# Performance work log

Hardware: AMD Instinct MI355X
Metric: run time of the kernel (lower is better)

## Reference

```python
import jax, jax.numpy as jnp
import numpy as np

N, NS, CIN, COUT, S = 65536, 16, 64, 64, 8
MID = COUT  # mid_planes = out_planes // 1
EPS = 1e-5


def _bn(t, g, b):
    # BatchNorm1d in training mode: normalize per channel over (points, neighbors)
    m = jnp.mean(t, axis=(0, 1), keepdims=True)
    v = jnp.var(t, axis=(0, 1), keepdims=True)
    return (t - m) * jax.lax.rsqrt(v + EPS) * g + b


def setup_inputs() -> dict:
    key = jax.random.key(0)
    ks = jax.random.split(key, 16)

    def w(k, shape, fan_in):
        return (jax.random.normal(k, shape, jnp.float32) / np.sqrt(fan_in)).astype(jnp.float32)

    return {
        "p": jax.random.uniform(ks[0], (N, 3), jnp.float32),
        "x": jax.random.normal(ks[1], (N, CIN), jnp.float32),
        "idx": jax.random.randint(ks[2], (N, NS), 0, N, jnp.int32),
        # q/k/v linears
        "Wq": w(ks[3], (CIN, MID), CIN), "bq": jnp.zeros((MID,), jnp.float32),
        "Wk": w(ks[4], (CIN, MID), CIN), "bk": jnp.zeros((MID,), jnp.float32),
        "Wv": w(ks[5], (CIN, COUT), CIN), "bv": jnp.zeros((COUT,), jnp.float32),
        # linear_p: Linear(3,3) -> BN(3) -> ReLU -> Linear(3,out)
        "Wp1": w(ks[6], (3, 3), 3), "bp1": jnp.zeros((3,), jnp.float32),
        "gp": jnp.ones((3,), jnp.float32), "bp_bn": jnp.zeros((3,), jnp.float32),
        "Wp2": w(ks[7], (3, COUT), 3), "bp2": jnp.zeros((COUT,), jnp.float32),
        # linear_w: BN(mid)->ReLU->Linear(mid,mid//s)->BN->ReLU->Linear(mid//s,mid//s)
        "gw1": jnp.ones((MID,), jnp.float32), "bw1_bn": jnp.zeros((MID,), jnp.float32),
        "Ww1": w(ks[8], (MID, MID // S), MID), "bw1": jnp.zeros((MID // S,), jnp.float32),
        "gw2": jnp.ones((MID // S,), jnp.float32), "bw2_bn": jnp.zeros((MID // S,), jnp.float32),
        "Ww2": w(ks[9], (MID // S, MID // S), MID // S), "bw2": jnp.zeros((MID // S,), jnp.float32),
    }


def reference(p, x, idx, Wq, bq, Wk, bk, Wv, bv, Wp1, bp1, gp, bp_bn, Wp2, bp2,
              gw1, bw1_bn, Ww1, bw1, gw2, bw2_bn, Ww2, bw2):
    # per-point projections
    xq = x @ Wq + bq                       # [N, MID]
    xk = x @ Wk + bk                       # [N, MID]
    xv = x @ Wv + bv                       # [N, COUT]
    # queryandgroup: gather neighbor features + relative xyz
    rel_p = p[idx] - p[:, None, :]         # [N, NS, 3]
    xk_g = xk[idx]                         # [N, NS, MID]
    xv_g = xv[idx]                         # [N, NS, COUT]
    # linear_p MLP on relative positions
    pr = rel_p @ Wp1 + bp1
    pr = jax.nn.relu(_bn(pr, gp, bp_bn))
    pr = pr @ Wp2 + bp2                    # [N, NS, COUT]
    # subtractive attention logits (out//mid == 1, so p_r sum is identity)
    w = xk_g - xq[:, None, :] + pr         # [N, NS, MID]
    # linear_w MLP
    w = jax.nn.relu(_bn(w, gw1, bw1_bn))
    w = w @ Ww1 + bw1                      # [N, NS, MID//S]
    w = jax.nn.relu(_bn(w, gw2, bw2_bn))
    w = w @ Ww2 + bw2                      # [N, NS, COUT//S]
    w = jax.nn.softmax(w, axis=1)          # softmax over neighbors
    # grouped weighted aggregation with shared attention planes
    n, ns, c = xv_g.shape
    out = ((xv_g + pr).reshape(n, ns, S, c // S) * w[:, :, None, :]).sum(1)
    return out.reshape(n, c)
```

## Files before the change

### kernel.cpp

```cpp
#include <hip/hip_runtime.h>

typedef unsigned short u16;
typedef __attribute__((ext_vector_type(8))) short bf16x8;
typedef __attribute__((ext_vector_type(2))) float f32x2;
typedef __attribute__((ext_vector_type(4))) float f32x4;

#define NPTS 65536
#define MTOT 1048576
#define M2TOT 131072
#define EPSb 1e-5f

#define XQ_OFF  0u
#define T_OFF   4194304u
#define ST_OFF  15728640u
#define XK_US   31457792u
#define XV_US   35652096u
#define WTQ_US  14680064u
#define WT1_US  14692352u

__device__ __forceinline__ float bf2f(u16 h) {
    return __uint_as_float(((unsigned)h) << 16);
}
__device__ __forceinline__ u16 f2bf(float f) {
    unsigned u = __float_as_uint(f);
    u += 0x7fffu + ((u >> 16) & 1u);
    return (u16)(u >> 16);
}
__device__ __forceinline__ unsigned cvt_pk_bf16(float lo, float hi) {
    unsigned r;
    asm("v_cvt_pk_bf16_f32 %0, %1, %2" : "=v"(r) : "v"(lo), "v"(hi));
    return r;
}
__device__ __forceinline__ bf16x8 pack_bf8(const float4 lo, const float4 hi) {
    union { bf16x8 v; unsigned u[4]; } r;
    r.u[0] = cvt_pk_bf16(lo.x, lo.y);
    r.u[1] = cvt_pk_bf16(lo.z, lo.w);
    r.u[2] = cvt_pk_bf16(hi.x, hi.y);
    r.u[3] = cvt_pk_bf16(hi.z, hi.w);
    return r.v;
}

struct BN2C {
    f32x2 A2[4], D[4], W0[4], W1[4], W2[4];
};
__device__ __forceinline__ void bn2c_build(
    BN2C& c, const int kbase, const float* __restrict__ ws,
    const float* __restrict__ gw1, const float* __restrict__ bw1_bn,
    const float* __restrict__ bp2, const float* __restrict__ Wp2)
{
    const float invM2 = 1.0f / (float)M2TOT;
#pragma unroll
    for (int j = 0; j < 4; ++j) {
        float a2[2], d[2], w0[2], w1[2], w2[2];
#pragma unroll
        for (int h = 0; h < 2; ++h) {
            const int k = kbase + 2 * j + h;
            const float mean = ws[ST_OFF + 6 + k] * invM2;
            const float var  = ws[ST_OFF + 70 + k] * invM2 - mean * mean;
            const float A2 = gw1[k] * rsqrtf(var + EPSb);
            const float B2 = bw1_bn[k] - mean * A2;
            a2[h] = A2; d[h] = fmaf(A2, bp2[k], B2);
            w0[h] = A2 * Wp2[k]; w1[h] = A2 * Wp2[64 + k]; w2[h] = A2 * Wp2[128 + k];
        }
        c.A2[j] = f32x2{a2[0], a2[1]}; c.D[j] = f32x2{d[0], d[1]};
        c.W0[j] = f32x2{w0[0], w0[1]}; c.W1[j] = f32x2{w1[0], w1[1]};
        c.W2[j] = f32x2{w2[0], w2[1]};
    }
}
__device__ __forceinline__ bf16x8 build_frag(
    const BN2C& c, const f32x2 t0v, const f32x2 t1v, const f32x2 t2v,
    const uint4 g, const float4 xlo, const float4 xhi)
{
    union { bf16x8 v; unsigned u[4]; } r;
    const unsigned gu[4] = { g.x, g.y, g.z, g.w };
    const f32x2 xp[4] = { {xlo.x, xlo.y}, {xlo.z, xlo.w}, {xhi.x, xhi.y}, {xhi.z, xhi.w} };
#pragma unroll
    for (int j = 0; j < 4; ++j) {
        f32x2 gf;
        gf.x = __uint_as_float(gu[j] << 16);
        gf.y = __uint_as_float(gu[j] & 0xffff0000u);
        f32x2 v = c.D[j] - c.A2[j] * xp[j];
        v = v + t0v * c.W0[j];
        v = v + t1v * c.W1[j];
        v = v + t2v * c.W2[j];
        v = v + c.A2[j] * gf;
        r.u[j] = cvt_pk_bf16(fmaxf(v.x, 0.0f), fmaxf(v.y, 0.0f));
    }
    return r.v;
}

__global__ __launch_bounds__(256) void k0_mom_tab(
    const float* __restrict__ p, const int* __restrict__ idx,
    const float* __restrict__ Wq, const float* __restrict__ Wk,
    const float* __restrict__ Wv, const float* __restrict__ Ww1,
    const float* __restrict__ Wp1, const float* __restrict__ bp1,
    float* __restrict__ ws)
{
    u16* wsu = (u16*)ws;
    __shared__ float sred[6];
    const int tid = threadIdx.x;
    const int gid = blockIdx.x * 256 + tid;
    if (tid < 6) sred[tid] = 0.0f;
    __syncthreads();

    if (gid < 12288) {
        const float* W = (gid < 4096) ? Wq : ((gid < 8192) ? Wk : Wv);
        const int rem = gid & 4095;
        const int n = rem >> 6, c = rem & 63;
        wsu[WTQ_US + (unsigned)gid] = f2bf(W[c * 64 + n]);
    } else if (gid < 12800) {
        const int rem = gid - 12288;
        const int c = rem >> 6, r = rem & 63;
        wsu[WT1_US + (unsigned)rem] = f2bf(Ww1[r * 8 + c]);
    }

    const int base = blockIdx.x * 128;
    const float w00 = Wp1[0], w01 = Wp1[1], w02 = Wp1[2];
    const float w10 = Wp1[3], w11 = Wp1[4], w12 = Wp1[5];
    const float w20 = Wp1[6], w21 = Wp1[7], w22 = Wp1[8];
    const float c0 = bp1[0], c1 = bp1[1], c2 = bp1[2];
    float s0 = 0, s1 = 0, s2 = 0, q0 = 0, q1 = 0, q2 = 0;
#pragma unroll
    for (int m = 0; m < 8; ++m) {
        const int pl = tid + m * 256;
        const int n  = base + (pl >> 4);
        const unsigned gpair = (unsigned)(base * 16 + pl);
        const int nb = idx[gpair];
        const float r0 = p[nb * 3 + 0] - p[n * 3 + 0];
        const float r1 = p[nb * 3 + 1] - p[n * 3 + 1];
        const float r2 = p[nb * 3 + 2] - p[n * 3 + 2];
        const float t0 = c0 + r0 * w00 + r1 * w10 + r2 * w20;
        const float t1 = c1 + r0 * w01 + r1 * w11 + r2 * w21;
        const float t2 = c2 + r0 * w02 + r1 * w12 + r2 * w22;
        s0 += t0; s1 += t1; s2 += t2;
        q0 += t0 * t0; q1 += t1 * t1; q2 += t2 * t2;
    }
    atomicAdd(&sred[0], s0); atomicAdd(&sred[1], s1); atomicAdd(&sred[2], s2);
    atomicAdd(&sred[3], q0); atomicAdd(&sred[4], q1); atomicAdd(&sred[5], q2);
    __syncthreads();
    if (tid < 6) atomicAdd(&ws[ST_OFF + tid], sred[tid]);
}

__global__ __launch_bounds__(256) void k1_proj(
    const float* __restrict__ p, const float* __restrict__ x, const int* __restrict__ idx,
    const float* __restrict__ bq, const float* __restrict__ bk, const float* __restrict__ bv,
    const float* __restrict__ Wp1, const float* __restrict__ bp1,
    const float* __restrict__ gp, const float* __restrict__ bp_bn,
    float* __restrict__ ws)
{
    u16* wsu = (u16*)ws;
    const int tid   = threadIdx.x;
    const int lane  = tid & 63;
    const int wid   = tid >> 6;
    const int col16 = lane & 15;
    const int quad  = lane >> 4;

    const float invM = 1.0f / (float)MTOT;
    float A1[3], B1[3];
#pragma unroll
    for (int a = 0; a < 3; ++a) {
        const float mean = ws[ST_OFF + a] * invM;
        const float var  = ws[ST_OFF + 3 + a] * invM - mean * mean;
        const float sc = gp[a] * rsqrtf(var + EPSb);
        A1[a] = sc; B1[a] = bp_bn[a] - mean * sc;
    }

    bf16x8 bf[3][4][2];
#pragma unroll
    for (int M = 0; M < 3; ++M)
#pragma unroll
        for (int t = 0; t < 4; ++t)
#pragma unroll
            for (int h = 0; h < 2; ++h)
                bf[M][t][h] = *(const bf16x8*)&wsu[WTQ_US +
                    (unsigned)(M * 4096 + (t * 16 + col16) * 64 + h * 32 + quad * 8)];

    float bq_t[4], bk_t[4], bv_t[4];
#pragma unroll
    for (int t = 0; t < 4; ++t) {
        bq_t[t] = bq[t * 16 + col16];
        bk_t[t] = bk[t * 16 + col16];
        bv_t[t] = bv[t * 16 + col16];
    }

    float* xq   = ws + XQ_OFF;
    u16*  xkb   = wsu + XK_US;
    u16*  xvb   = wsu + XV_US;

    const int gw = blockIdx.x * 4 + wid;
#pragma unroll
    for (int g = 0; g < 2; ++g) {
        const int n0 = (gw * 2 + g) * 16;
        const float* xrow = x + (unsigned)(n0 + col16) * 64u;
        const float4 fa0 = *(const float4*)&xrow[quad * 8];
        const float4 fa1 = *(const float4*)&xrow[quad * 8 + 4];
        const float4 fb0 = *(const float4*)&xrow[32 + quad * 8];
        const float4 fb1 = *(const float4*)&xrow[32 + quad * 8 + 4];
        const bf16x8 a0 = pack_bf8(fa0, fa1);
        const bf16x8 a1 = pack_bf8(fb0, fb1);

#pragma unroll
        for (int t = 0; t < 4; ++t) {
            f32x4 aq = {0,0,0,0}, ak = {0,0,0,0}, av = {0,0,0,0};
            aq = __builtin_amdgcn_mfma_f32_16x16x32_bf16(a0, bf[0][t][0], aq, 0, 0, 0);
            aq = __builtin_amdgcn_mfma_f32_16x16x32_bf16(a1, bf[0][t][1], aq, 0, 0, 0);
            ak = __builtin_amdgcn_mfma_f32_16x16x32_bf16(a0, bf[1][t][0], ak, 0, 0, 0);
            ak = __builtin_amdgcn_mfma_f32_16x16x32_bf16(a1, bf[1][t][1], ak, 0, 0, 0);
            av = __builtin_amdgcn_mfma_f32_16x16x32_bf16(a0, bf[2][t][0], av, 0, 0, 0);
            av = __builtin_amdgcn_mfma_f32_16x16x32_bf16(a1, bf[2][t][1], av, 0, 0, 0);
#pragma unroll
            for (int r = 0; r < 4; ++r) {
                const unsigned row = (unsigned)(n0 + quad * 4 + r);
                const unsigned o   = row * 64u + (unsigned)(t * 16 + col16);
                xq[o]  = aq[r] + bq_t[t];
                xkb[o] = f2bf(ak[r] + bk_t[t]);
                xvb[o] = f2bf(av[r] + bv_t[t]);
            }
        }
    }

    const int base = blockIdx.x * 128;
    const float w00 = Wp1[0], w01 = Wp1[1], w02 = Wp1[2];
    const float w10 = Wp1[3], w11 = Wp1[4], w12 = Wp1[5];
    const float w20 = Wp1[6], w21 = Wp1[7], w22 = Wp1[8];
    const float c0 = bp1[0], c1 = bp1[1], c2 = bp1[2];
#pragma unroll
    for (int m = 0; m < 8; ++m) {
        const int pl = tid + m * 256;
        const int n  = base + (pl >> 4);
        const unsigned gpair = (unsigned)(base * 16 + pl);
        const int nb = idx[gpair];
        const float r0 = p[nb * 3 + 0] - p[n * 3 + 0];
        const float r1 = p[nb * 3 + 1] - p[n * 3 + 1];
        const float r2 = p[nb * 3 + 2] - p[n * 3 + 2];
        const float t0 = c0 + r0 * w00 + r1 * w10 + r2 * w20;
        const float t1 = c1 + r0 * w01 + r1 * w11 + r2 * w21;
        const float t2 = c2 + r0 * w02 + r1 * w12 + r2 * w22;
        ws[T_OFF + gpair * 3u + 0u] = fmaxf(fmaf(t0, A1[0], B1[0]), 0.0f);
        ws[T_OFF + gpair * 3u + 1u] = fmaxf(fmaf(t1, A1[1], B1[1]), 0.0f);
        ws[T_OFF + gpair * 3u + 2u] = fmaxf(fmaf(t2, A1[2], B1[2]), 0.0f);
    }
}

__global__ __launch_bounds__(256) void k2_bn2(
    const int* __restrict__ idx,
    const float* __restrict__ Wp2, const float* __restrict__ bp2,
    float* __restrict__ ws)
{
    u16* wsu = (u16*)ws;
    __shared__ float ss[64], sq[64];
    const int tid = threadIdx.x;
    const int lane = tid & 63;
    const int gw = blockIdx.x * 4 + (tid >> 6);
    if (tid < 64) { ss[tid] = 0.0f; sq[tid] = 0.0f; }

    const float wp20 = Wp2[lane], wp21 = Wp2[64 + lane], wp22 = Wp2[128 + lane];
    const float bp2c = bp2[lane];
    const float* xq  = ws + XQ_OFF;
    const float* T   = ws + T_OFF;
    const u16*  xkb  = wsu + XK_US;

    float s = 0.0f, q = 0.0f;

    for (int nn = 0; nn < 4; ++nn) {
        const int nu = __builtin_amdgcn_readfirstlane((gw * 4 + nn) * 8);

        const int4* ir4 = (const int4*)(idx + (unsigned)nu * 16u);
        const int4 i0 = ir4[0], i1 = ir4[1], i2 = ir4[2], i3 = ir4[3];
        const int nbs[16] = { i0.x, i0.y, i0.z, i0.w, i1.x, i1.y, i1.z, i1.w,
                              i2.x, i2.y, i2.z, i2.w, i3.x, i3.y, i3.z, i3.w };
        u16 kr[16];
#pragma unroll
        for (int j = 0; j < 16; ++j) kr[j] = xkb[(unsigned)nbs[j] * 64u + lane];

        float tr[48];
        const float4* Tr4 = (const float4*)(T + (unsigned)nu * 48u);
#pragma unroll
        for (int c = 0; c < 12; ++c) {
            const float4 v = Tr4[c];
            tr[4 * c + 0] = v.x; tr[4 * c + 1] = v.y;
            tr[4 * c + 2] = v.z; tr[4 * c + 3] = v.w;
        }
        const float xqc  = xq[(unsigned)nu * 64u + lane];
        const float base = bp2c - xqc;

#pragma unroll
        for (int j = 0; j < 16; ++j) {
            const float prx = base + tr[3 * j + 0] * wp20
                                   + tr[3 * j + 1] * wp21
                                   + tr[3 * j + 2] * wp22;
            const float w0 = bf2f(kr[j]) + prx;
            s += w0; q = fmaf(w0, w0, q);
        }
    }
    __syncthreads();
    atomicAdd(&ss[lane], s); atomicAdd(&sq[lane], q);
    __syncthreads();
    if (tid < 64) {
        atomicAdd(&ws[ST_OFF + 6 + tid], ss[tid]);
        atomicAdd(&ws[ST_OFF + 70 + tid], sq[tid]);
    }
}

__global__ __launch_bounds__(256) void k2b_bn3(
    const int* __restrict__ idx,
    const float* __restrict__ Wp2, const float* __restrict__ bp2,
    const float* __restrict__ gw1, const float* __restrict__ bw1_bn,
    const float* __restrict__ bw1,
    float* __restrict__ ws)
{
    u16* wsu = (u16*)ws;
    __shared__ float s3r[8], q3r[8];
    const int tid   = threadIdx.x;
    const int lane  = tid & 63;
    const int wid   = tid >> 6;
    const int col16 = lane & 15;
    const int quad  = lane >> 4;
    if (tid < 8) { s3r[tid] = 0.0f; q3r[tid] = 0.0f; }
    __syncthreads();

    BN2C cA, cB;
    bn2c_build(cA, quad * 8,      ws, gw1, bw1_bn, bp2, Wp2);
    bn2c_build(cB, 32 + quad * 8, ws, gw1, bw1_bn, bp2, Wp2);

    bf16x8 b0 = {0,0,0,0,0,0,0,0}, b1 = {0,0,0,0,0,0,0,0};
    if (col16 < 8) {
        b0 = *(const bf16x8*)&wsu[WT1_US + (unsigned)(col16 * 64 + quad * 8)];
        b1 = *(const bf16x8*)&wsu[WT1_US + (unsigned)(col16 * 64 + 32 + quad * 8)];
    }
    const float bw1c = (col16 < 8) ? bw1[col16] : 0.0f;

    const float* xq  = ws + XQ_OFF;
    const float* T   = ws + T_OFF;
    const u16*  xkb  = wsu + XK_US;
    const int sg = (blockIdx.x * 4 + wid) * 8;
    float bs = 0.0f, bq2 = 0.0f;

    for (int it = 0; it < 8; ++it) {
        const int nu = __builtin_amdgcn_readfirstlane((sg + it) * 8);

        const int nbv = idx[(unsigned)nu * 16u + (unsigned)col16];
        const u16* grow = xkb + (unsigned)nbv * 64u;
        const uint4 gA = *(const uint4*)(grow + quad * 8);
        const uint4 gB = *(const uint4*)(grow + 32 + quad * 8);

        const float* Trow = T + (unsigned)nu * 48u + (unsigned)col16 * 3u;
        const f32x2 t0v = f32x2{Trow[0], Trow[0]};
        const f32x2 t1v = f32x2{Trow[1], Trow[1]};
        const f32x2 t2v = f32x2{Trow[2], Trow[2]};

        const float* xr = xq + (unsigned)nu * 64u;
        const float4 x0 = *(const float4*)(xr + quad * 8);
        const float4 x1 = *(const float4*)(xr + quad * 8 + 4);
        const float4 x2 = *(const float4*)(xr + 32 + quad * 8);
        const float4 x3 = *(const float4*)(xr + 32 + quad * 8 + 4);

        const bf16x8 a0 = build_frag(cA, t0v, t1v, t2v, gA, x0, x1);
        const bf16x8 a1 = build_frag(cB, t0v, t1v, t2v, gB, x2, x3);

        f32x4 acc = {0.0f, 0.0f, 0.0f, 0.0f};
        acc = __builtin_amdgcn_mfma_f32_16x16x32_bf16(a0, b0, acc, 0, 0, 0);
        acc = __builtin_amdgcn_mfma_f32_16x16x32_bf16(a1, b1, acc, 0, 0, 0);
        if (col16 < 8) {
#pragma unroll
            for (int r = 0; r < 4; ++r) {
                const float o = acc[r] + bw1c;
                bs += o;
                bq2 = fmaf(o, o, bq2);
            }
        }
    }
    if (col16 < 8) {
        atomicAdd(&s3r[col16], bs);
        atomicAdd(&q3r[col16], bq2);
    }
    __syncthreads();
    if (tid < 8) {
        atomicAdd(&ws[ST_OFF + 134 + tid], s3r[tid]);
        atomicAdd(&ws[ST_OFF + 142 + tid], q3r[tid]);
    }
}

__global__ __launch_bounds__(256) void k34_fused(
    const int* __restrict__ idx,
    const float* __restrict__ Wp2, const float* __restrict__ bp2,
    const float* __restrict__ gw1, const float* __restrict__ bw1_bn,
    const float* __restrict__ bw1,
    const float* __restrict__ gw2, const float* __restrict__ bw2_bn,
    const float* __restrict__ Ww2, const float* __restrict__ bw2,
    const float* __restrict__ ws, float* __restrict__ out)
{
    const u16* wsu = (const u16*)ws;
    __shared__ float sv3[4][16][8];
    __shared__ float se[4][16][8];
    const int tid   = threadIdx.x;
    const int lane  = tid & 63;
    const int wid   = tid >> 6;
    const int col16 = lane & 15;
    const int quad  = lane >> 4;
    const int tt    = lane & 7;
    const int j1    = lane >> 3;

    const float invM2 = 1.0f / (float)M2TOT;
    BN2C cA, cB;
    bn2c_build(cA, quad * 8,      ws, gw1, bw1_bn, bp2, Wp2);
    bn2c_build(cB, 32 + quad * 8, ws, gw1, bw1_bn, bp2, Wp2);

    bf16x8 b0 = {0,0,0,0,0,0,0,0}, b1 = {0,0,0,0,0,0,0,0};
    if (col16 < 8) {
        b0 = *(const bf16x8*)&wsu[WT1_US + (unsigned)(col16 * 64 + quad * 8)];
        b1 = *(const bf16x8*)&wsu[WT1_US + (unsigned)(col16 * 64 + 32 + quad * 8)];
    }
    const float bw1c = (col16 < 8) ? bw1[col16] : 0.0f;
    const int   c3    = col16 & 7;
    const float mean3 = ws[ST_OFF + 134 + c3] * invM2;
    const float var3  = ws[ST_OFF + 142 + c3] * invM2 - mean3 * mean3;
    const float A3c   = gw2[c3] * rsqrtf(var3 + EPSb);
    const float B3f   = fmaf(A3c, bw1c, bw2_bn[c3] - mean3 * A3c);
    float ww2c[8];
#pragma unroll
    for (int u = 0; u < 8; ++u) ww2c[u] = Ww2[u * 8 + tt];
    const float bw2c = bw2[tt];
    const float wp20 = Wp2[lane], wp21 = Wp2[64 + lane], wp22 = Wp2[128 + lane];
    const float bp2c = bp2[lane];

    const float* xq  = ws + XQ_OFF;
    const float* T   = ws + T_OFF;
    const u16*  xkb  = wsu + XK_US;
    const u16*  xvb  = wsu + XV_US;

    const int n0 = (blockIdx.x * 4 + wid) * 16;
    for (int it = 0; it < 16; ++it) {
        const int nu = __builtin_amdgcn_readfirstlane(n0 + it);

        const int4* ir4 = (const int4*)(idx + (unsigned)nu * 16u);
        const int4 i0 = ir4[0], i1 = ir4[1], i2 = ir4[2], i3 = ir4[3];
        const int nbs[16] = { i0.x, i0.y, i0.z, i0.w, i1.x, i1.y, i1.z, i1.w,
                              i2.x, i2.y, i2.z, i2.w, i3.x, i3.y, i3.z, i3.w };
        const int nbv = idx[(unsigned)nu * 16u + (unsigned)col16];
        const u16* grow = xkb + (unsigned)nbv * 64u;
        const uint4 gA = *(const uint4*)(grow + quad * 8);
        const uint4 gB = *(const uint4*)(grow + 32 + quad * 8);
        u16 xvr[16];
#pragma unroll
        for (int j = 0; j < 16; ++j) xvr[j] = xvb[(unsigned)nbs[j] * 64u + lane];

        const float* Trow = T + (unsigned)nu * 48u + (unsigned)col16 * 3u;
        const f32x2 t0v = f32x2{Trow[0], Trow[0]};
        const f32x2 t1v = f32x2{Trow[1], Trow[1]};
        const f32x2 t2v = f32x2{Trow[2], Trow[2]};
        float tr[48];
        const float4* Tr4 = (const float4*)(T + (unsigned)nu * 48u);
#pragma unroll
        for (int c = 0; c < 12; ++c) {
            const float4 v = Tr4[c];
            tr[4 * c + 0] = v.x; tr[4 * c + 1] = v.y;
            tr[4 * c + 2] = v.z; tr[4 * c + 3] = v.w;
        }
        const float* xr = xq + (unsigned)nu * 64u;
        const float4 x0 = *(const float4*)(xr + quad * 8);
        const float4 x1 = *(const float4*)(xr + quad * 8 + 4);
        const float4 x2 = *(const float4*)(xr + 32 + quad * 8);
        const float4 x3 = *(const float4*)(xr + 32 + quad * 8 + 4);

        const bf16x8 a0 = build_frag(cA, t0v, t1v, t2v, gA, x0, x1);
        const bf16x8 a1 = build_frag(cB, t0v, t1v, t2v, gB, x2, x3);

        f32x4 acc = {0.0f, 0.0f, 0.0f, 0.0f};
        acc = __builtin_amdgcn_mfma_f32_16x16x32_bf16(a0, b0, acc, 0, 0, 0);
        acc = __builtin_amdgcn_mfma_f32_16x16x32_bf16(a1, b1, acc, 0, 0, 0);

        if (col16 < 8) {
#pragma unroll
            for (int r = 0; r < 4; ++r)
                sv3[wid][quad * 4 + r][col16] = fmaxf(fmaf(A3c, acc[r], B3f), 0.0f);
        }
        float s0 = bw2c, s1 = bw2c;
#pragma unroll
        for (int u = 0; u < 8; ++u) {
            s0 = fmaf(sv3[wid][j1][u], ww2c[u], s0);
            s1 = fmaf(sv3[wid][j1 + 8][u], ww2c[u], s1);
        }
        float mx = fmaxf(s0, s1);
        mx = fmaxf(mx, __shfl_xor(mx, 8));
        mx = fmaxf(mx, __shfl_xor(mx, 16));
        mx = fmaxf(mx, __shfl_xor(mx, 32));
        const float e0 = __expf(s0 - mx);
        const float e1 = __expf(s1 - mx);
        float sm = e0 + e1;
        sm += __shfl_xor(sm, 8);
        sm += __shfl_xor(sm, 16);
        sm += __shfl_xor(sm, 32);
        const float rs = __builtin_amdgcn_rcpf(sm);
        se[wid][j1][tt]     = e0 * rs;
        se[wid][j1 + 8][tt] = e1 * rs;

        float xvacc = 0.0f, ta0 = 0.0f, ta1 = 0.0f, ta2 = 0.0f;
#pragma unroll
        for (int j = 0; j < 16; ++j) {
            const float ej = se[wid][j][tt];
            xvacc = fmaf(bf2f(xvr[j]), ej, xvacc);
            ta0 = fmaf(tr[3 * j + 0], ej, ta0);
            ta1 = fmaf(tr[3 * j + 1], ej, ta1);
            ta2 = fmaf(tr[3 * j + 2], ej, ta2);
        }
        out[(unsigned)nu * 64u + lane] =
            fmaf(ta0, wp20, fmaf(ta1, wp21, fmaf(ta2, wp22, xvacc + bp2c)));
    }
}

extern "C" void kernel_launch(void* const* d_in, const int* in_sizes, int n_in,
                              void* d_out, int out_size, void* d_ws, size_t ws_size,
                              hipStream_t stream)
{
    const float* p      = (const float*)d_in[0];
    const float* x      = (const float*)d_in[1];
    const int*   idx    = (const int*)d_in[2];
    const float* Wq     = (const float*)d_in[3];
    const float* bq     = (const float*)d_in[4];
    const float* Wk     = (const float*)d_in[5];
    const float* bk     = (const float*)d_in[6];
    const float* Wv     = (const float*)d_in[7];
    const float* bv     = (const float*)d_in[8];
    const float* Wp1    = (const float*)d_in[9];
    const float* bp1    = (const float*)d_in[10];
    const float* gp     = (const float*)d_in[11];
    const float* bp_bn  = (const float*)d_in[12];
    const float* Wp2    = (const float*)d_in[13];
    const float* bp2    = (const float*)d_in[14];
    const float* gw1    = (const float*)d_in[15];
    const float* bw1_bn = (const float*)d_in[16];
    const float* Ww1    = (const float*)d_in[17];
    const float* bw1    = (const float*)d_in[18];
    const float* gw2    = (const float*)d_in[19];
    const float* bw2_bn = (const float*)d_in[20];
    const float* Ww2    = (const float*)d_in[21];
    const float* bw2    = (const float*)d_in[22];
    float* ws  = (float*)d_ws;
    float* out = (float*)d_out;
    (void)in_sizes; (void)n_in; (void)out_size; (void)ws_size;

    hipMemsetAsync((char*)d_ws + (size_t)ST_OFF * 4, 0, 150 * sizeof(float), stream);

    k0_mom_tab<<<512, 256, 0, stream>>>(p, idx, Wq, Wk, Wv, Ww1, Wp1, bp1, ws);
    k1_proj<<<512, 256, 0, stream>>>(p, x, idx, bq, bk, bv, Wp1, bp1, gp, bp_bn, ws);
    k2_bn2<<<512, 256, 0, stream>>>(idx, Wp2, bp2, ws);
    k2b_bn3<<<256, 256, 0, stream>>>(idx, Wp2, bp2, gw1, bw1_bn, bw1, ws);
    k34_fused<<<1024, 256, 0, stream>>>(idx, Wp2, bp2, gw1, bw1_bn, bw1,
                                        gw2, bw2_bn, Ww2, bw2, ws, out);
}
```

Before: 253.0 us.

## Software-pipeline neighbor gathers and replace LDS softmax exchange with shuffles

The fused attention loop now prefetches the next point's gathered key/value rows, position table entries and query row while the current point is computed. Neighbor indices are loaded two iterations ahead. The shared-memory buffer for the normalized softmax weights is dropped; weights are broadcast with cross-lane shuffles and the relative-position weighted sums are reduced with xor shuffles instead of reading the full 48-float table per lane. This targets gather latency and LDS traffic, at the cost of higher register pressure and some redundant wrap-around prefetches at block ends.

```diff
diff --git a/kernel.cpp b/kernel.cpp
--- a/kernel.cpp
+++ b/kernel.cpp
@@ -87,6 +87,14 @@
         r.u[j] = cvt_pk_bf16(fmaxf(v.x, 0.0f), fmaxf(v.y, 0.0f));
     }
     return r.v;
+}
+__device__ __forceinline__ bf16x8 build_frag8(
+    const BN2C& c, const f32x2 t0v, const f32x2 t1v, const f32x2 t2v,
+    const uint4 g, const float* xp8)
+{
+    const float4 xlo = {xp8[0], xp8[1], xp8[2], xp8[3]};
+    const float4 xhi = {xp8[4], xp8[5], xp8[6], xp8[7]};
+    return build_frag(c, t0v, t1v, t2v, g, xlo, xhi);
 }
 
 __global__ __launch_bounds__(256) void k0_mom_tab(
@@ -392,7 +400,6 @@
 {
     const u16* wsu = (const u16*)ws;
     __shared__ float sv3[4][16][8];
-    __shared__ float se[4][16][8];
     const int tid   = threadIdx.x;
     const int lane  = tid & 63;
     const int wid   = tid >> 6;
@@ -430,45 +437,81 @@
     const u16*  xvb  = wsu + XV_US;
 
     const int n0 = (blockIdx.x * 4 + wid) * 16;
-    for (int it = 0; it < 16; ++it) {
-        const int nu = __builtin_amdgcn_readfirstlane(n0 + it);
-
-        const int4* ir4 = (const int4*)(idx + (unsigned)nu * 16u);
-        const int4 i0 = ir4[0], i1 = ir4[1], i2 = ir4[2], i3 = ir4[3];
-        const int nbs[16] = { i0.x, i0.y, i0.z, i0.w, i1.x, i1.y, i1.z, i1.w,
-                              i2.x, i2.y, i2.z, i2.w, i3.x, i3.y, i3.z, i3.w };
-        const int nbv = idx[(unsigned)nu * 16u + (unsigned)col16];
+
+    int   nbs[16];
+    int   nbv;
+    uint4 gA, gB;
+    u16   xvr[16];
+    float t0, t1, t2;
+    float xqA[8], xqB[8];
+
+    {
+        const unsigned nu = (unsigned)n0;
+        const int4* ir4 = (const int4*)(idx + nu * 16u);
+        int4 i0 = ir4[0], i1 = ir4[1], i2 = ir4[2], i3 = ir4[3];
+        nbs[0]=i0.x; nbs[1]=i0.y; nbs[2]=i0.z; nbs[3]=i0.w;
+        nbs[4]=i1.x; nbs[5]=i1.y; nbs[6]=i1.z; nbs[7]=i1.w;
+        nbs[8]=i2.x; nbs[9]=i2.y; nbs[10]=i2.z; nbs[11]=i2.w;
+        nbs[12]=i3.x; nbs[13]=i3.y; nbs[14]=i3.z; nbs[15]=i3.w;
+        nbv = idx[nu * 16u + (unsigned)col16];
         const u16* grow = xkb + (unsigned)nbv * 64u;
-        const uint4 gA = *(const uint4*)(grow + quad * 8);
-        const uint4 gB = *(const uint4*)(grow + 32 + quad * 8);
-        u16 xvr[16];
+        gA = *(const uint4*)(grow + quad * 8);
+        gB = *(const uint4*)(grow + 32 + quad * 8);
 #pragma unroll
         for (int j = 0; j < 16; ++j) xvr[j] = xvb[(unsigned)nbs[j] * 64u + lane];
-
-        const float* Trow = T + (unsigned)nu * 48u + (unsigned)col16 * 3u;
-        const f32x2 t0v = f32x2{Trow[0], Trow[0]};
-        const f32x2 t1v = f32x2{Trow[1], Trow[1]};
-        const f32x2 t2v = f32x2{Trow[2], Trow[2]};
-        float tr[48];
-        const float4* Tr4 = (const float4*)(T + (unsigned)nu * 48u);
-#pragma unroll
-        for (int c = 0; c < 12; ++c) {
-            const float4 v = Tr4[c];
-            tr[4 * c + 0] = v.x; tr[4 * c + 1] = v.y;
-            tr[4 * c + 2] = v.z; tr[4 * c + 3] = v.w;
-        }
-        const float* xr = xq + (unsigned)nu * 64u;
+        const float* Trow = T + nu * 48u + (unsigned)col16 * 3u;
+        t0 = Trow[0]; t1 = Trow[1]; t2 = Trow[2];
+        const float* xr = xq + nu * 64u;
         const float4 x0 = *(const float4*)(xr + quad * 8);
         const float4 x1 = *(const float4*)(xr + quad * 8 + 4);
         const float4 x2 = *(const float4*)(xr + 32 + quad * 8);
         const float4 x3 = *(const float4*)(xr + 32 + quad * 8 + 4);
-
-        const bf16x8 a0 = build_frag(cA, t0v, t1v, t2v, gA, x0, x1);
-        const bf16x8 a1 = build_frag(cB, t0v, t1v, t2v, gB, x2, x3);
-
+        xqA[0]=x0.x; xqA[1]=x0.y; xqA[2]=x0.z; xqA[3]=x0.w;
+        xqA[4]=x1.x; xqA[5]=x1.y; xqA[6]=x1.z; xqA[7]=x1.w;
+        xqB[0]=x2.x; xqB[1]=x2.y; xqB[2]=x2.z; xqB[3]=x2.w;
+        xqB[4]=x3.x; xqB[5]=x3.y; xqB[6]=x3.z; xqB[7]=x3.w;
+        const unsigned nu1 = (nu + 1u) & 65535u;
+        const int4* jr4 = (const int4*)(idx + nu1 * 16u);
+        i0 = jr4[0]; i1 = jr4[1]; i2 = jr4[2]; i3 = jr4[3];
+        nbs[0]=i0.x; nbs[1]=i0.y; nbs[2]=i0.z; nbs[3]=i0.w;
+        nbs[4]=i1.x; nbs[5]=i1.y; nbs[6]=i1.z; nbs[7]=i1.w;
+        nbs[8]=i2.x; nbs[9]=i2.y; nbs[10]=i2.z; nbs[11]=i2.w;
+        nbs[12]=i3.x; nbs[13]=i3.y; nbs[14]=i3.z; nbs[15]=i3.w;
+        nbv = idx[nu1 * 16u + (unsigned)col16];
+    }
+
+    for (int it = 0; it < 16; ++it) {
+        const unsigned nu = (unsigned)(n0 + it);
+
+        const f32x2 t0v = f32x2{t0, t0};
+        const f32x2 t1v = f32x2{t1, t1};
+        const f32x2 t2v = f32x2{t2, t2};
+        const bf16x8 a0 = build_frag8(cA, t0v, t1v, t2v, gA, xqA);
+        const bf16x8 a1 = build_frag8(cB, t0v, t1v, t2v, gB, xqB);
         f32x4 acc = {0.0f, 0.0f, 0.0f, 0.0f};
         acc = __builtin_amdgcn_mfma_f32_16x16x32_bf16(a0, b0, acc, 0, 0, 0);
         acc = __builtin_amdgcn_mfma_f32_16x16x32_bf16(a1, b1, acc, 0, 0, 0);
+
+        const float tA0 = __shfl(t0, j1),     tA1 = __shfl(t1, j1),     tA2 = __shfl(t2, j1);
+        const float tB0 = __shfl(t0, j1 + 8), tB1 = __shfl(t1, j1 + 8), tB2 = __shfl(t2, j1 + 8);
+
+        const unsigned nu1 = (nu + 1u) & 65535u;
+        {
+            const u16* grow = xkb + (unsigned)nbv * 64u;
+            gA = *(const uint4*)(grow + quad * 8);
+            gB = *(const uint4*)(grow + 32 + quad * 8);
+            const float* Trow = T + nu1 * 48u + (unsigned)col16 * 3u;
+            t0 = Trow[0]; t1 = Trow[1]; t2 = Trow[2];
+            const float* xr = xq + nu1 * 64u;
+            const float4 x0 = *(const float4*)(xr + quad * 8);
+            const float4 x1 = *(const float4*)(xr + quad * 8 + 4);
+            const float4 x2 = *(const float4*)(xr + 32 + quad * 8);
+            const float4 x3 = *(const float4*)(xr + 32 + quad * 8 + 4);
+            xqA[0]=x0.x; xqA[1]=x0.y; xqA[2]=x0.z; xqA[3]=x0.w;
+            xqA[4]=x1.x; xqA[5]=x1.y; xqA[6]=x1.z; xqA[7]=x1.w;
+            xqB[0]=x2.x; xqB[1]=x2.y; xqB[2]=x2.z; xqB[3]=x2.w;
+            xqB[4]=x3.x; xqB[5]=x3.y; xqB[6]=x3.z; xqB[7]=x3.w;
+        }
 
         if (col16 < 8) {
 #pragma unroll
@@ -492,20 +535,37 @@
         sm += __shfl_xor(sm, 16);
         sm += __shfl_xor(sm, 32);
         const float rs = __builtin_amdgcn_rcpf(sm);
-        se[wid][j1][tt]     = e0 * rs;
-        se[wid][j1 + 8][tt] = e1 * rs;
-
-        float xvacc = 0.0f, ta0 = 0.0f, ta1 = 0.0f, ta2 = 0.0f;
-#pragma unroll
-        for (int j = 0; j < 16; ++j) {
-            const float ej = se[wid][j][tt];
-            xvacc = fmaf(bf2f(xvr[j]), ej, xvacc);
-            ta0 = fmaf(tr[3 * j + 0], ej, ta0);
-            ta1 = fmaf(tr[3 * j + 1], ej, ta1);
-            ta2 = fmaf(tr[3 * j + 2], ej, ta2);
-        }
-        out[(unsigned)nu * 64u + lane] =
-            fmaf(ta0, wp20, fmaf(ta1, wp21, fmaf(ta2, wp22, xvacc + bp2c)));
+        const float e0n = e0 * rs, e1n = e1 * rs;
+
+        float xvacc = 0.0f;
+#pragma unroll
+        for (int j = 0; j < 8; ++j) {
+            const int src = (j << 3) | tt;
+            const float ejl = __shfl(e0n, src);
+            const float ejh = __shfl(e1n, src);
+            xvacc = fmaf(bf2f(xvr[j]),     ejl, xvacc);
+            xvacc = fmaf(bf2f(xvr[j + 8]), ejh, xvacc);
+        }
+        float r0 = fmaf(e0n, tA0, e1n * tB0);
+        float r1 = fmaf(e0n, tA1, e1n * tB1);
+        float r2 = fmaf(e0n, tA2, e1n * tB2);
+        r0 += __shfl_xor(r0, 8); r0 += __shfl_xor(r0, 16); r0 += __shfl_xor(r0, 32);
+        r1 += __shfl_xor(r1, 8); r1 += __shfl_xor(r1, 16); r1 += __shfl_xor(r1, 32);
+        r2 += __shfl_xor(r2, 8); r2 += __shfl_xor(r2, 16); r2 += __shfl_xor(r2, 32);
+        out[nu * 64u + lane] =
+            fmaf(r0, wp20, fmaf(r1, wp21, fmaf(r2, wp22, xvacc + bp2c)));
+
+#pragma unroll
+        for (int j = 0; j < 16; ++j) xvr[j] = xvb[(unsigned)nbs[j] * 64u + lane];
+
+        const unsigned nu2 = (nu + 2u) & 65535u;
+        const int4* ir4 = (const int4*)(idx + nu2 * 16u);
+        const int4 i0 = ir4[0], i1 = ir4[1], i2 = ir4[2], i3 = ir4[3];
+        nbs[0]=i0.x; nbs[1]=i0.y; nbs[2]=i0.z; nbs[3]=i0.w;
+        nbs[4]=i1.x; nbs[5]=i1.y; nbs[6]=i1.z; nbs[7]=i1.w;
+        nbs[8]=i2.x; nbs[9]=i2.y; nbs[10]=i2.z; nbs[11]=i2.w;
+        nbs[12]=i3.x; nbs[13]=i3.y; nbs[14]=i3.z; nbs[15]=i3.w;
+        nbv = idx[nu2 * 16u + (unsigned)col16];
     }
 }
 
```

Result: no change. 257.1 us (+1.6%).
